# Kernel tuning notes

Hardware: AMD Instinct MI355X
Metric: run time of the kernel (lower is better)

## Reference

```python
import math
import jax, jax.numpy as jnp
import numpy as np

B, L, IN_DIM, D, OUT_DIM = 4, 4096, 512, 64, 512


def setup_inputs() -> dict:
    key = jax.random.key(0)
    ks = jax.random.split(key, 9)
    s_in = 1.0 / math.sqrt(IN_DIM)
    s_d = 1.0 / math.sqrt(D)
    return {
        "x": jax.random.normal(ks[0], (B, L, IN_DIM), jnp.float32),
        "Wq": jax.random.normal(ks[1], (IN_DIM, D), jnp.float32) * s_in,
        "bq": jax.random.normal(ks[2], (D,), jnp.float32) * s_in,
        "Wk": jax.random.normal(ks[3], (IN_DIM, D), jnp.float32) * s_in,
        "bk": jax.random.normal(ks[4], (D,), jnp.float32) * s_in,
        "Wv": jax.random.normal(ks[5], (IN_DIM, D), jnp.float32) * s_in,
        "bv": jax.random.normal(ks[6], (D,), jnp.float32) * s_in,
        "Wo": jax.random.normal(ks[7], (D, OUT_DIM), jnp.float32) * s_d,
        "bo": jax.random.normal(ks[8], (OUT_DIM,), jnp.float32) * s_d,
    }


def reference(x, Wq, bq, Wk, bk, Wv, bv, Wo, bo):
    # q, k, v: [B, L, D]
    q = x @ Wq + bq
    k = x @ Wk + bk
    v = x @ Wv + bv
    scale = 1.0 / math.sqrt(D)
    # scores: [B, Lq, Lk]
    scores = jnp.einsum("bqd,bkd->bqk", q, k) * scale
    # NOTE: original uses nn.Softmax(dim=1) -> softmax over the QUERY axis (axis=1)
    attention = jax.nn.softmax(scores, axis=1)
    values_with_attention = jnp.einsum("bqk,bkd->bqd", attention, v)
    output = values_with_attention @ Wo + bo
    return (output, attention)
```

## Files before the change

### kernel.cpp

```cpp
#include <hip/hip_runtime.h>
#include <hip/hip_fp16.h>
#include <math.h>

#define Bdim 4
#define Lseq 4096
#define INDIM 512
#define DH 64
#define OUTD 512
#define SCALE 0.125f
#define KSPL 8
#define QSPL 4
#define BL (Bdim * Lseq)

typedef _Float16 f16;
typedef _Float16 h8 __attribute__((ext_vector_type(8)));
typedef float f4 __attribute__((ext_vector_type(4)));

#define MFMA(a, b, c) __builtin_amdgcn_mfma_f32_16x16x32_f16(a, b, c, 0, 0, 0)

__global__ __launch_bounds__(256) void proj_h(const float* __restrict__ x,
                                              const float* __restrict__ W,
                                              const float* __restrict__ bias,
                                              f16* __restrict__ out, float scale) {
    __shared__ float xT[64 * 68];
    __shared__ float Ws[64 * 68];
    int t = threadIdx.x;
    int row0 = blockIdx.x * 64;
    int r4 = t >> 4;
    int c4 = t & 15;
    float acc[4][4] = {};
    for (int kc = 0; kc < INDIM; kc += 64) {
        __syncthreads();
        {
            int row = t >> 2, kq = (t & 3) * 16;
            const float4* src = (const float4*)(x + (size_t)(row0 + row) * INDIM + kc + kq);
            float tmp[16];
#pragma unroll
            for (int i = 0; i < 4; ++i) {
                float4 v = src[i];
                tmp[4*i+0] = v.x; tmp[4*i+1] = v.y; tmp[4*i+2] = v.z; tmp[4*i+3] = v.w;
            }
#pragma unroll
            for (int j = 0; j < 16; ++j) xT[(kq + j) * 68 + row] = tmp[j];
        }
        {
            int k = t >> 2, dq = (t & 3) * 16;
            const float4* src = (const float4*)(W + (size_t)(kc + k) * DH + dq);
#pragma unroll
            for (int i = 0; i < 4; ++i)
                *(float4*)(Ws + k * 68 + dq + 4 * i) = src[i];
        }
        __syncthreads();
#pragma unroll 8
        for (int k = 0; k < 64; ++k) {
            f4 xv = *(f4*)(xT + k * 68 + r4 * 4);
            f4 wv = *(f4*)(Ws + k * 68 + c4 * 4);
#pragma unroll
            for (int i = 0; i < 4; ++i)
#pragma unroll
                for (int j = 0; j < 4; ++j) acc[i][j] += xv[i] * wv[j];
        }
    }
#pragma unroll
    for (int i = 0; i < 4; ++i) {
        size_t row = row0 + r4 * 4 + i;
#pragma unroll
        for (int j = 0; j < 4; ++j) {
            int d = c4 * 4 + j;
            out[row * DH + d] = (f16)((acc[i][j] + bias[d]) * scale);
        }
    }
}

__global__ __launch_bounds__(256) void proj_f(const float* __restrict__ x,
                                              const float* __restrict__ W,
                                              const float* __restrict__ bias,
                                              float* __restrict__ out) {
    __shared__ float xT[64 * 68];
    __shared__ float Ws[64 * 68];
    int t = threadIdx.x;
    int row0 = blockIdx.x * 64;
    int r4 = t >> 4, c4 = t & 15;
    float acc[4][4] = {};
    for (int kc = 0; kc < INDIM; kc += 64) {
        __syncthreads();
        {
            int row = t >> 2, kq = (t & 3) * 16;
            const float4* src = (const float4*)(x + (size_t)(row0 + row) * INDIM + kc + kq);
            float tmp[16];
#pragma unroll
            for (int i = 0; i < 4; ++i) {
                float4 v = src[i];
                tmp[4*i+0] = v.x; tmp[4*i+1] = v.y; tmp[4*i+2] = v.z; tmp[4*i+3] = v.w;
            }
#pragma unroll
            for (int j = 0; j < 16; ++j) xT[(kq + j) * 68 + row] = tmp[j];
        }
        {
            int k = t >> 2, dq = (t & 3) * 16;
            const float4* src = (const float4*)(W + (size_t)(kc + k) * DH + dq);
#pragma unroll
            for (int i = 0; i < 4; ++i)
                *(float4*)(Ws + k * 68 + dq + 4 * i) = src[i];
        }
        __syncthreads();
#pragma unroll 8
        for (int k = 0; k < 64; ++k) {
            f4 xv = *(f4*)(xT + k * 68 + r4 * 4);
            f4 wv = *(f4*)(Ws + k * 68 + c4 * 4);
#pragma unroll
            for (int i = 0; i < 4; ++i)
#pragma unroll
                for (int j = 0; j < 4; ++j) acc[i][j] += xv[i] * wv[j];
        }
    }
#pragma unroll
    for (int i = 0; i < 4; ++i) {
        size_t row = row0 + r4 * 4 + i;
#pragma unroll
        for (int j = 0; j < 4; ++j) {
            int d = c4 * 4 + j;
            out[row * DH + d] = acc[i][j] + bias[d];
        }
    }
}

__global__ __launch_bounds__(256) void vtrans(const float* __restrict__ v32,
                                              f16* __restrict__ vt) {
    __shared__ float tile[64 * 65];
    int t = threadIdx.x;
    int b = blockIdx.y, k0 = blockIdx.x * 64;
#pragma unroll
    for (int i = 0; i < 4; ++i) {
        int lin = i * 256 + t;
        int row = lin >> 4, c4 = (lin & 15) * 4;
        float4 v = *(const float4*)(v32 + ((size_t)b * Lseq + k0 + row) * DH + c4);
        tile[row * 65 + c4 + 0] = v.x;
        tile[row * 65 + c4 + 1] = v.y;
        tile[row * 65 + c4 + 2] = v.z;
        tile[row * 65 + c4 + 3] = v.w;
    }
    __syncthreads();
    int d = t >> 2, kq = (t & 3) * 16;
#pragma unroll
    for (int i = 0; i < 2; ++i) {
        h8 pack;
#pragma unroll
        for (int j = 0; j < 8; ++j) pack[j] = (f16)tile[(kq + i * 8 + j) * 65 + d];
        *(h8*)(vt + ((size_t)b * DH + d) * Lseq + k0 + kq + i * 8) = pack;
    }
}

__global__ __launch_bounds__(256) void col_stats(const f16* __restrict__ qh,
                                                 const f16* __restrict__ kh,
                                                 float* __restrict__ lsum) {
    __shared__ __align__(16) f16 qlds[32 * 72];
    int t = threadIdx.x;
    int w = t >> 6, lane = t & 63;
    int l15 = lane & 15, quad = lane >> 4;
    int b = blockIdx.y;
    int kblk = blockIdx.x * 64;
    int qbase = blockIdx.z * (Lseq / QSPL);

    int krow = kblk + w * 16 + l15;
    const h8* kr = (const h8*)(kh + ((size_t)b * Lseq + krow) * DH + quad * 8);
    h8 a0 = kr[0];
    h8 a1 = kr[4];
    float lp[4] = {0.f, 0.f, 0.f, 0.f};

    for (int qs = 0; qs < Lseq / QSPL; qs += 32) {
        __syncthreads();
        {
            int row = t >> 3, c8 = t & 7;
            *(h8*)(qlds + row * 72 + c8 * 8) =
                *(const h8*)(qh + ((size_t)b * Lseq + qbase + qs + row) * DH + c8 * 8);
        }
        __syncthreads();
#pragma unroll
        for (int nt = 0; nt < 2; ++nt) {
            const f16* qp = qlds + (nt * 16 + l15) * 72 + quad * 8;
            h8 b0 = *(const h8*)qp;
            h8 b1 = *(const h8*)(qp + 32);
            f4 c = {0.f, 0.f, 0.f, 0.f};
            c = MFMA(a0, b0, c);
            c = MFMA(a1, b1, c);
#pragma unroll
            for (int reg = 0; reg < 4; ++reg) lp[reg] += __expf(c[reg]);
        }
    }
#pragma unroll
    for (int reg = 0; reg < 4; ++reg) {
        float v = lp[reg];
        v += __shfl_xor(v, 1);
        v += __shfl_xor(v, 2);
        v += __shfl_xor(v, 4);
        v += __shfl_xor(v, 8);
        if (l15 == 0)
            atomicAdd(&lsum[(size_t)b * Lseq + kblk + w * 16 + quad * 4 + reg], v);
    }
}

__global__ __launch_bounds__(256) void rlk(const float* __restrict__ lsum,
                                           float* __restrict__ rl) {
    int i = blockIdx.x * 256 + threadIdx.x;
    rl[i] = 1.0f / lsum[i];
}

__global__ __launch_bounds__(256) void attn_pv(const f16* __restrict__ qh,
                                               const f16* __restrict__ kh,
                                               const f16* __restrict__ vt,
                                               const float* __restrict__ rl,
                                               float* __restrict__ att,
                                               f16* __restrict__ opart) {
    __shared__ __align__(16) f16 klds[64 * 72];
    __shared__ __align__(16) f16 elds[4][32 * 80];
    int t = threadIdx.x;
    int w = t >> 6, lane = t & 63;
    int l15 = lane & 15, quad = lane >> 4;
    int b = blockIdx.y;
    int q0 = blockIdx.x * 128 + w * 32;
    int split = blockIdx.z;

    h8 aq[2][2];
#pragma unroll
    for (int mt = 0; mt < 2; ++mt) {
        const h8* qp = (const h8*)(qh + ((size_t)b * Lseq + q0 + mt * 16 + l15) * DH + quad * 8);
        aq[mt][0] = qp[0];
        aq[mt][1] = qp[4];
    }
    f4 o[2][4];
#pragma unroll
    for (int mt = 0; mt < 2; ++mt)
#pragma unroll
        for (int nt = 0; nt < 4; ++nt) o[mt][nt] = (f4){0.f, 0.f, 0.f, 0.f};

    const float* rlb = rl + (size_t)b * Lseq;
    f16* ew = elds[w];

    for (int kt = 0; kt < Lseq / KSPL; kt += 64) {
        int kbase = split * (Lseq / KSPL) + kt;
        __syncthreads();
#pragma unroll
        for (int i = 0; i < 2; ++i) {
            int lin = i * 256 + t;
            int row = lin >> 3, c8 = lin & 7;
            *(h8*)(klds + row * 72 + c8 * 8) =
                *(const h8*)(kh + ((size_t)b * Lseq + kbase + row) * DH + c8 * 8);
        }
        __syncthreads();

        h8 bk[4][2];
        float rlv[4];
#pragma unroll
        for (int nt = 0; nt < 4; ++nt) {
            const f16* kp = klds + (nt * 16 + l15) * 72 + quad * 8;
            bk[nt][0] = *(const h8*)kp;
            bk[nt][1] = *(const h8*)(kp + 32);
            rlv[nt] = rlb[kbase + nt * 16 + l15];
        }

#pragma unroll
        for (int mt = 0; mt < 2; ++mt)
#pragma unroll
            for (int nt = 0; nt < 4; ++nt) {
                f4 c = {0.f, 0.f, 0.f, 0.f};
                c = MFMA(aq[mt][0], bk[nt][0], c);
                c = MFMA(aq[mt][1], bk[nt][1], c);
#pragma unroll
                for (int reg = 0; reg < 4; ++reg) {
                    float a = __expf(c[reg]) * rlv[nt];
                    int qrow = mt * 16 + quad * 4 + reg;
                    att[((size_t)b * Lseq + q0 + qrow) * Lseq + kbase + nt * 16 + l15] = a;
                    ew[qrow * 80 + nt * 16 + l15] = (f16)a;
                }
            }

        h8 ae[2][2];
#pragma unroll
        for (int mt = 0; mt < 2; ++mt) {
            const f16* ep = ew + (mt * 16 + l15) * 80 + quad * 8;
            ae[mt][0] = *(const h8*)ep;
            ae[mt][1] = *(const h8*)(ep + 32);
        }
#pragma unroll
        for (int nt = 0; nt < 4; ++nt) {
            const h8* vp = (const h8*)(vt + ((size_t)b * DH + nt * 16 + l15) * Lseq + kbase + quad * 8);
            h8 bv0 = vp[0];
            h8 bv1 = vp[4];
            o[0][nt] = MFMA(ae[0][0], bv0, o[0][nt]);
            o[0][nt] = MFMA(ae[0][1], bv1, o[0][nt]);
            o[1][nt] = MFMA(ae[1][0], bv0, o[1][nt]);
            o[1][nt] = MFMA(ae[1][1], bv1, o[1][nt]);
        }
    }

#pragma unroll
    for (int mt = 0; mt < 2; ++mt)
#pragma unroll
        for (int nt = 0; nt < 4; ++nt)
#pragma unroll
            for (int reg = 0; reg < 4; ++reg) {
                size_t qrow = (size_t)b * Lseq + q0 + mt * 16 + quad * 4 + reg;
                opart[((size_t)split * BL + qrow) * DH + nt * 16 + l15] = (f16)o[mt][nt][reg];
            }
}

__global__ __launch_bounds__(256) void out_proj(const f16* __restrict__ opart,
                                                const float* __restrict__ Wo,
                                                const float* __restrict__ bo,
                                                float* __restrict__ out) {
    __shared__ float os[16 * DH];
    __shared__ float wos[DH * 128];
    int t = threadIdx.x;
    int rg = blockIdx.x, oq = blockIdx.y;
#pragma unroll
    for (int j = 0; j < 32; ++j) {
        int idx = j * 256 + t;
        int dd = idx >> 7, oo = idx & 127;
        wos[idx] = Wo[(size_t)dd * OUTD + oq * 128 + oo];
    }
#pragma unroll
    for (int j = 0; j < 4; ++j) {
        int idx = j * 256 + t;
        size_t R = (size_t)rg * 16 + (idx >> 6);
        int dd = idx & 63;
        float s = 0.f;
#pragma unroll
        for (int sp = 0; sp < KSPL; ++sp)
            s += (float)opart[((size_t)sp * BL + R) * DH + dd];
        os[idx] = s;
    }
    __syncthreads();
    int ol = t & 127, rp = t >> 7;
    float bias = bo[oq * 128 + ol];
#pragma unroll
    for (int j = 0; j < 8; ++j) {
        int rr = rp * 8 + j;
        float acc = bias;
#pragma unroll 16
        for (int dd = 0; dd < DH; ++dd) acc += os[rr * DH + dd] * wos[dd * 128 + ol];
        out[((size_t)rg * 16 + rr) * OUTD + oq * 128 + ol] = acc;
    }
}

extern "C" void kernel_launch(void* const* d_in, const int* in_sizes, int n_in,
                              void* d_out, int out_size, void* d_ws, size_t ws_size,
                              hipStream_t stream) {
    const float* x  = (const float*)d_in[0];
    const float* Wq = (const float*)d_in[1];
    const float* bq = (const float*)d_in[2];
    const float* Wk = (const float*)d_in[3];
    const float* bk = (const float*)d_in[4];
    const float* Wv = (const float*)d_in[5];
    const float* bv = (const float*)d_in[6];
    const float* Wo = (const float*)d_in[7];
    const float* bo = (const float*)d_in[8];

    float* out = (float*)d_out;
    float* att = out + (size_t)BL * OUTD;

    char* ws = (char*)d_ws;
    f16*   qh    = (f16*)(ws + 0);
    f16*   kh    = (f16*)(ws + (size_t)(2 << 20));
    float* v32   = (float*)(ws + (size_t)(4 << 20));
    f16*   vt    = (f16*)(ws + (size_t)(8 << 20));
    float* lsum  = (float*)(ws + (size_t)(10 << 20));
    float* rlw   = (float*)(ws + (size_t)(10 << 20) + (1 << 16));
    f16*   opart = (f16*)(ws + (size_t)(11 << 20));

    proj_h<<<dim3(BL / 64), 256, 0, stream>>>(x, Wq, bq, qh, SCALE);
    proj_h<<<dim3(BL / 64), 256, 0, stream>>>(x, Wk, bk, kh, 1.0f);
    proj_f<<<dim3(BL / 64), 256, 0, stream>>>(x, Wv, bv, v32);
    vtrans<<<dim3(Lseq / 64, Bdim), 256, 0, stream>>>(v32, vt);
    hipMemsetAsync(lsum, 0, (size_t)BL * sizeof(float), stream);
    col_stats<<<dim3(Lseq / 64, Bdim, QSPL), 256, 0, stream>>>(qh, kh, lsum);
    rlk<<<dim3(BL / 256), 256, 0, stream>>>(lsum, rlw);
    attn_pv<<<dim3(Lseq / 128, Bdim, KSPL), 256, 0, stream>>>(qh, kh, vt, rlw, att, opart);
    out_proj<<<dim3(BL / 16, 4), 256, 0, stream>>>(opart, Wo, bo, out);
}
```

Baseline: 522.4 us.

## Fuse QKV projection into one MFMA kernel, use exp2 and MFMA output projection

Replaces the three scalar fp32 projection kernels with a single fp16 MFMA kernel that reads x once and computes Q, K and V together, using transposed fp16 weight copies. Folds log2(e) into the Q scale so exp2f replaces __expf. Drops the LDS staging of K in attn_pv and col_stats. Swaps the operand order so attention rows are written as float4 stores. Also converts the output projection to MFMA and sums the split partials in fp16. The cost is extra small weight-transpose launches and more fp16 rounding in the projections and the partial reduction.

New measurement: 523.0 us. About the same (+0.1%).

```diff
diff --git a/kernel.cpp b/kernel.cpp
--- a/kernel.cpp
+++ b/kernel.cpp
@@ -1,5 +1,4 @@
 #include <hip/hip_runtime.h>
-#include <hip/hip_fp16.h>
 #include <math.h>
 
 #define Bdim 4
@@ -7,196 +6,139 @@
 #define INDIM 512
 #define DH 64
 #define OUTD 512
-#define SCALE 0.125f
 #define KSPL 8
 #define QSPL 4
 #define BL (Bdim * Lseq)
+#define QS 0.18033688011112042f
 
 typedef _Float16 f16;
 typedef _Float16 h8 __attribute__((ext_vector_type(8)));
+typedef _Float16 h4 __attribute__((ext_vector_type(4)));
 typedef float f4 __attribute__((ext_vector_type(4)));
 
 #define MFMA(a, b, c) __builtin_amdgcn_mfma_f32_16x16x32_f16(a, b, c, 0, 0, 0)
 
-__global__ __launch_bounds__(256) void proj_h(const float* __restrict__ x,
-                                              const float* __restrict__ W,
-                                              const float* __restrict__ bias,
-                                              f16* __restrict__ out, float scale) {
-    __shared__ float xT[64 * 68];
-    __shared__ float Ws[64 * 68];
+__global__ __launch_bounds__(256) void transpose_w(const float* __restrict__ W,
+                                                   f16* __restrict__ WT,
+                                                   int K, int N, float scale) {
+    int id = blockIdx.x * 256 + threadIdx.x;
+    if (id >= K * N) return;
+    int n = id / K, k = id % K;
+    WT[(size_t)n * K + k] = (f16)(W[(size_t)k * N + n] * scale);
+}
+
+__global__ __launch_bounds__(256) void qkvh(const float* __restrict__ x,
+                                            const f16* __restrict__ WqT,
+                                            const f16* __restrict__ WkT,
+                                            const f16* __restrict__ WvT,
+                                            const float* __restrict__ bq,
+                                            const float* __restrict__ bk,
+                                            const float* __restrict__ bv,
+                                            f16* __restrict__ qh,
+                                            f16* __restrict__ kh,
+                                            f16* __restrict__ vh) {
+    __shared__ __align__(16) f16 xh[64 * 136];
     int t = threadIdx.x;
-    int row0 = blockIdx.x * 64;
-    int r4 = t >> 4;
-    int c4 = t & 15;
-    float acc[4][4] = {};
-    for (int kc = 0; kc < INDIM; kc += 64) {
+    int w = t >> 6, lane = t & 63, l15 = lane & 15, quad = lane >> 4;
+    size_t row0 = (size_t)blockIdx.x * 64;
+
+    f4 acc[12];
+#pragma unroll
+    for (int i = 0; i < 12; ++i) acc[i] = (f4){0.f, 0.f, 0.f, 0.f};
+
+    const f16* wbase[12];
+#pragma unroll
+    for (int nt = 0; nt < 12; ++nt) {
+        const f16* Wt = nt < 4 ? WqT : (nt < 8 ? WkT : WvT);
+        wbase[nt] = Wt + (size_t)((nt & 3) * 16 + l15) * INDIM + quad * 8;
+    }
+
+    int xr = t >> 2, xc = (t & 3) * 4;
+    for (int kc = 0; kc < INDIM; kc += 128) {
         __syncthreads();
-        {
-            int row = t >> 2, kq = (t & 3) * 16;
-            const float4* src = (const float4*)(x + (size_t)(row0 + row) * INDIM + kc + kq);
-            float tmp[16];
-#pragma unroll
-            for (int i = 0; i < 4; ++i) {
-                float4 v = src[i];
-                tmp[4*i+0] = v.x; tmp[4*i+1] = v.y; tmp[4*i+2] = v.z; tmp[4*i+3] = v.w;
+#pragma unroll
+        for (int i = 0; i < 8; ++i) {
+            float4 v = *(const float4*)(x + (row0 + xr) * INDIM + kc + xc + i * 16);
+            h4 p = {(f16)v.x, (f16)v.y, (f16)v.z, (f16)v.w};
+            *(h4*)(xh + xr * 136 + xc + i * 16) = p;
+        }
+        __syncthreads();
+#pragma unroll
+        for (int ks = 0; ks < 4; ++ks) {
+            h8 a = *(const h8*)(xh + (w * 16 + l15) * 136 + ks * 32 + quad * 8);
+#pragma unroll
+            for (int nt = 0; nt < 12; ++nt) {
+                h8 bf = *(const h8*)(wbase[nt] + kc + ks * 32);
+                acc[nt] = MFMA(a, bf, acc[nt]);
             }
-#pragma unroll
-            for (int j = 0; j < 16; ++j) xT[(kq + j) * 68 + row] = tmp[j];
-        }
-        {
-            int k = t >> 2, dq = (t & 3) * 16;
-            const float4* src = (const float4*)(W + (size_t)(kc + k) * DH + dq);
-#pragma unroll
-            for (int i = 0; i < 4; ++i)
-                *(float4*)(Ws + k * 68 + dq + 4 * i) = src[i];
-        }
-        __syncthreads();
-#pragma unroll 8
-        for (int k = 0; k < 64; ++k) {
-            f4 xv = *(f4*)(xT + k * 68 + r4 * 4);
-            f4 wv = *(f4*)(Ws + k * 68 + c4 * 4);
-#pragma unroll
-            for (int i = 0; i < 4; ++i)
-#pragma unroll
-                for (int j = 0; j < 4; ++j) acc[i][j] += xv[i] * wv[j];
-        }
-    }
-#pragma unroll
-    for (int i = 0; i < 4; ++i) {
-        size_t row = row0 + r4 * 4 + i;
-#pragma unroll
-        for (int j = 0; j < 4; ++j) {
-            int d = c4 * 4 + j;
-            out[row * DH + d] = (f16)((acc[i][j] + bias[d]) * scale);
-        }
-    }
-}
-
-__global__ __launch_bounds__(256) void proj_f(const float* __restrict__ x,
-                                              const float* __restrict__ W,
-                                              const float* __restrict__ bias,
-                                              float* __restrict__ out) {
-    __shared__ float xT[64 * 68];
-    __shared__ float Ws[64 * 68];
-    int t = threadIdx.x;
-    int row0 = blockIdx.x * 64;
-    int r4 = t >> 4, c4 = t & 15;
-    float acc[4][4] = {};
-    for (int kc = 0; kc < INDIM; kc += 64) {
-        __syncthreads();
-        {
-            int row = t >> 2, kq = (t & 3) * 16;
-            const float4* src = (const float4*)(x + (size_t)(row0 + row) * INDIM + kc + kq);
-            float tmp[16];
-#pragma unroll
-            for (int i = 0; i < 4; ++i) {
-                float4 v = src[i];
-                tmp[4*i+0] = v.x; tmp[4*i+1] = v.y; tmp[4*i+2] = v.z; tmp[4*i+3] = v.w;
-            }
-#pragma unroll
-            for (int j = 0; j < 16; ++j) xT[(kq + j) * 68 + row] = tmp[j];
-        }
-        {
-            int k = t >> 2, dq = (t & 3) * 16;
-            const float4* src = (const float4*)(W + (size_t)(kc + k) * DH + dq);
-#pragma unroll
-            for (int i = 0; i < 4; ++i)
-                *(float4*)(Ws + k * 68 + dq + 4 * i) = src[i];
-        }
-        __syncthreads();
-#pragma unroll 8
-        for (int k = 0; k < 64; ++k) {
-            f4 xv = *(f4*)(xT + k * 68 + r4 * 4);
-            f4 wv = *(f4*)(Ws + k * 68 + c4 * 4);
-#pragma unroll
-            for (int i = 0; i < 4; ++i)
-#pragma unroll
-                for (int j = 0; j < 4; ++j) acc[i][j] += xv[i] * wv[j];
-        }
-    }
-#pragma unroll
-    for (int i = 0; i < 4; ++i) {
-        size_t row = row0 + r4 * 4 + i;
-#pragma unroll
-        for (int j = 0; j < 4; ++j) {
-            int d = c4 * 4 + j;
-            out[row * DH + d] = acc[i][j] + bias[d];
-        }
-    }
-}
-
-__global__ __launch_bounds__(256) void vtrans(const float* __restrict__ v32,
+        }
+    }
+#pragma unroll
+    for (int nt = 0; nt < 12; ++nt) {
+        int n = (nt & 3) * 16 + l15;
+        f16* dst;
+        float bias;
+        if (nt < 4)      { dst = qh; bias = bq[n] * QS; }
+        else if (nt < 8) { dst = kh; bias = bk[n]; }
+        else             { dst = vh; bias = bv[n]; }
+#pragma unroll
+        for (int r = 0; r < 4; ++r) {
+            size_t row = row0 + w * 16 + quad * 4 + r;
+            dst[row * DH + n] = (f16)(acc[nt][r] + bias);
+        }
+    }
+}
+
+__global__ __launch_bounds__(256) void vtrans(const f16* __restrict__ vh,
                                               f16* __restrict__ vt) {
-    __shared__ float tile[64 * 65];
+    __shared__ __align__(16) f16 tile[64 * 72];
     int t = threadIdx.x;
     int b = blockIdx.y, k0 = blockIdx.x * 64;
-#pragma unroll
-    for (int i = 0; i < 4; ++i) {
-        int lin = i * 256 + t;
-        int row = lin >> 4, c4 = (lin & 15) * 4;
-        float4 v = *(const float4*)(v32 + ((size_t)b * Lseq + k0 + row) * DH + c4);
-        tile[row * 65 + c4 + 0] = v.x;
-        tile[row * 65 + c4 + 1] = v.y;
-        tile[row * 65 + c4 + 2] = v.z;
-        tile[row * 65 + c4 + 3] = v.w;
-    }
+    int row = t >> 2, c16 = (t & 3) * 16;
+    const h8* src = (const h8*)(vh + ((size_t)b * Lseq + k0 + row) * DH + c16);
+    *(h8*)(tile + row * 72 + c16) = src[0];
+    *(h8*)(tile + row * 72 + c16 + 8) = src[1];
     __syncthreads();
     int d = t >> 2, kq = (t & 3) * 16;
 #pragma unroll
     for (int i = 0; i < 2; ++i) {
-        h8 pack;
-#pragma unroll
-        for (int j = 0; j < 8; ++j) pack[j] = (f16)tile[(kq + i * 8 + j) * 65 + d];
-        *(h8*)(vt + ((size_t)b * DH + d) * Lseq + k0 + kq + i * 8) = pack;
+        h8 p;
+#pragma unroll
+        for (int j = 0; j < 8; ++j) p[j] = tile[(kq + i * 8 + j) * 72 + d];
+        *(h8*)(vt + ((size_t)b * DH + d) * Lseq + k0 + kq + i * 8) = p;
     }
 }
 
 __global__ __launch_bounds__(256) void col_stats(const f16* __restrict__ qh,
                                                  const f16* __restrict__ kh,
                                                  float* __restrict__ lsum) {
-    __shared__ __align__(16) f16 qlds[32 * 72];
-    int t = threadIdx.x;
-    int w = t >> 6, lane = t & 63;
-    int l15 = lane & 15, quad = lane >> 4;
+    int t = threadIdx.x, w = t >> 6, lane = t & 63, l15 = lane & 15, quad = lane >> 4;
     int b = blockIdx.y;
-    int kblk = blockIdx.x * 64;
-    int qbase = blockIdx.z * (Lseq / QSPL);
-
-    int krow = kblk + w * 16 + l15;
-    const h8* kr = (const h8*)(kh + ((size_t)b * Lseq + krow) * DH + quad * 8);
-    h8 a0 = kr[0];
-    h8 a1 = kr[4];
-    float lp[4] = {0.f, 0.f, 0.f, 0.f};
-
-    for (int qs = 0; qs < Lseq / QSPL; qs += 32) {
-        __syncthreads();
-        {
-            int row = t >> 3, c8 = t & 7;
-            *(h8*)(qlds + row * 72 + c8 * 8) =
-                *(const h8*)(qh + ((size_t)b * Lseq + qbase + qs + row) * DH + c8 * 8);
-        }
-        __syncthreads();
-#pragma unroll
-        for (int nt = 0; nt < 2; ++nt) {
-            const f16* qp = qlds + (nt * 16 + l15) * 72 + quad * 8;
-            h8 b0 = *(const h8*)qp;
-            h8 b1 = *(const h8*)(qp + 32);
-            f4 c = {0.f, 0.f, 0.f, 0.f};
-            c = MFMA(a0, b0, c);
-            c = MFMA(a1, b1, c);
-#pragma unroll
-            for (int reg = 0; reg < 4; ++reg) lp[reg] += __expf(c[reg]);
-        }
-    }
-#pragma unroll
-    for (int reg = 0; reg < 4; ++reg) {
-        float v = lp[reg];
+    int k16 = blockIdx.x * 64 + w * 16;
+    size_t qbase = (size_t)blockIdx.z * (Lseq / QSPL);
+
+    const h8* kr = (const h8*)(kh + ((size_t)b * Lseq + k16 + l15) * DH + quad * 8);
+    h8 a0 = kr[0], a1 = kr[4];
+    f4 lp = {0.f, 0.f, 0.f, 0.f};
+    const f16* qb = qh + ((size_t)b * Lseq + qbase) * DH;
+#pragma unroll 4
+    for (int q = 0; q < Lseq / QSPL; q += 16) {
+        const h8* qr = (const h8*)(qb + (size_t)(q + l15) * DH + quad * 8);
+        h8 b0 = qr[0], b1 = qr[4];
+        f4 c = {0.f, 0.f, 0.f, 0.f};
+        c = MFMA(a0, b0, c);
+        c = MFMA(a1, b1, c);
+#pragma unroll
+        for (int r = 0; r < 4; ++r) lp[r] += exp2f(c[r]);
+    }
+#pragma unroll
+    for (int r = 0; r < 4; ++r) {
+        float v = lp[r];
         v += __shfl_xor(v, 1);
         v += __shfl_xor(v, 2);
         v += __shfl_xor(v, 4);
         v += __shfl_xor(v, 8);
-        if (l15 == 0)
-            atomicAdd(&lsum[(size_t)b * Lseq + kblk + w * 16 + quad * 4 + reg], v);
+        if (l15 == 0) atomicAdd(&lsum[(size_t)b * Lseq + k16 + quad * 4 + r], v);
     }
 }
 
@@ -212,21 +154,17 @@
                                                const float* __restrict__ rl,
                                                float* __restrict__ att,
                                                f16* __restrict__ opart) {
-    __shared__ __align__(16) f16 klds[64 * 72];
-    __shared__ __align__(16) f16 elds[4][32 * 80];
-    int t = threadIdx.x;
-    int w = t >> 6, lane = t & 63;
-    int l15 = lane & 15, quad = lane >> 4;
-    int b = blockIdx.y;
+    __shared__ __align__(16) f16 ew[4][32 * 72];
+    int t = threadIdx.x, w = t >> 6, lane = t & 63, l15 = lane & 15, quad = lane >> 4;
+    int b = blockIdx.y, split = blockIdx.z;
     int q0 = blockIdx.x * 128 + w * 32;
-    int split = blockIdx.z;
-
-    h8 aq[2][2];
+
+    h8 bq[2][2];
 #pragma unroll
     for (int mt = 0; mt < 2; ++mt) {
         const h8* qp = (const h8*)(qh + ((size_t)b * Lseq + q0 + mt * 16 + l15) * DH + quad * 8);
-        aq[mt][0] = qp[0];
-        aq[mt][1] = qp[4];
+        bq[mt][0] = qp[0];
+        bq[mt][1] = qp[4];
     }
     f4 o[2][4];
 #pragma unroll
@@ -234,112 +172,95 @@
 #pragma unroll
         for (int nt = 0; nt < 4; ++nt) o[mt][nt] = (f4){0.f, 0.f, 0.f, 0.f};
 
+    f16* e = ew[w];
+    const f16* khb = kh + (size_t)b * Lseq * DH;
+    const f16* vtb = vt + (size_t)b * DH * Lseq;
     const float* rlb = rl + (size_t)b * Lseq;
-    f16* ew = elds[w];
+    float* attb = att + ((size_t)b * Lseq + q0) * Lseq;
 
     for (int kt = 0; kt < Lseq / KSPL; kt += 64) {
-        int kbase = split * (Lseq / KSPL) + kt;
-        __syncthreads();
-#pragma unroll
-        for (int i = 0; i < 2; ++i) {
-            int lin = i * 256 + t;
-            int row = lin >> 3, c8 = lin & 7;
-            *(h8*)(klds + row * 72 + c8 * 8) =
-                *(const h8*)(kh + ((size_t)b * Lseq + kbase + row) * DH + c8 * 8);
-        }
-        __syncthreads();
-
-        h8 bk[4][2];
-        float rlv[4];
+        int kb = split * (Lseq / KSPL) + kt;
+        h8 ak[4][2];
+        f4 rlv[4];
 #pragma unroll
         for (int nt = 0; nt < 4; ++nt) {
-            const f16* kp = klds + (nt * 16 + l15) * 72 + quad * 8;
-            bk[nt][0] = *(const h8*)kp;
-            bk[nt][1] = *(const h8*)(kp + 32);
-            rlv[nt] = rlb[kbase + nt * 16 + l15];
-        }
-
+            const h8* kp = (const h8*)(khb + (size_t)(kb + nt * 16 + l15) * DH + quad * 8);
+            ak[nt][0] = kp[0];
+            ak[nt][1] = kp[4];
+            rlv[nt] = *(const f4*)(rlb + kb + nt * 16 + quad * 4);
+        }
 #pragma unroll
         for (int mt = 0; mt < 2; ++mt)
 #pragma unroll
             for (int nt = 0; nt < 4; ++nt) {
                 f4 c = {0.f, 0.f, 0.f, 0.f};
-                c = MFMA(aq[mt][0], bk[nt][0], c);
-                c = MFMA(aq[mt][1], bk[nt][1], c);
-#pragma unroll
-                for (int reg = 0; reg < 4; ++reg) {
-                    float a = __expf(c[reg]) * rlv[nt];
-                    int qrow = mt * 16 + quad * 4 + reg;
-                    att[((size_t)b * Lseq + q0 + qrow) * Lseq + kbase + nt * 16 + l15] = a;
-                    ew[qrow * 80 + nt * 16 + l15] = (f16)a;
+                c = MFMA(ak[nt][0], bq[mt][0], c);
+                c = MFMA(ak[nt][1], bq[mt][1], c);
+                f4 av;
+                h4 ah;
+#pragma unroll
+                for (int r = 0; r < 4; ++r) {
+                    float a = exp2f(c[r]) * rlv[nt][r];
+                    av[r] = a;
+                    ah[r] = (f16)a;
                 }
+                *(f4*)(attb + (size_t)(mt * 16 + l15) * Lseq + kb + nt * 16 + quad * 4) = av;
+                *(h4*)(e + (mt * 16 + l15) * 72 + nt * 16 + quad * 4) = ah;
             }
-
         h8 ae[2][2];
 #pragma unroll
         for (int mt = 0; mt < 2; ++mt) {
-            const f16* ep = ew + (mt * 16 + l15) * 80 + quad * 8;
+            const f16* ep = e + (mt * 16 + l15) * 72 + quad * 8;
             ae[mt][0] = *(const h8*)ep;
             ae[mt][1] = *(const h8*)(ep + 32);
         }
 #pragma unroll
         for (int nt = 0; nt < 4; ++nt) {
-            const h8* vp = (const h8*)(vt + ((size_t)b * DH + nt * 16 + l15) * Lseq + kbase + quad * 8);
-            h8 bv0 = vp[0];
-            h8 bv1 = vp[4];
-            o[0][nt] = MFMA(ae[0][0], bv0, o[0][nt]);
-            o[0][nt] = MFMA(ae[0][1], bv1, o[0][nt]);
-            o[1][nt] = MFMA(ae[1][0], bv0, o[1][nt]);
-            o[1][nt] = MFMA(ae[1][1], bv1, o[1][nt]);
-        }
-    }
-
+            const h8* vp = (const h8*)(vtb + (size_t)(nt * 16 + l15) * Lseq + kb + quad * 8);
+            h8 b0 = vp[0], b1 = vp[4];
+#pragma unroll
+            for (int mt = 0; mt < 2; ++mt) {
+                o[mt][nt] = MFMA(ae[mt][0], b0, o[mt][nt]);
+                o[mt][nt] = MFMA(ae[mt][1], b1, o[mt][nt]);
+            }
+        }
+    }
 #pragma unroll
     for (int mt = 0; mt < 2; ++mt)
 #pragma unroll
         for (int nt = 0; nt < 4; ++nt)
 #pragma unroll
-            for (int reg = 0; reg < 4; ++reg) {
-                size_t qrow = (size_t)b * Lseq + q0 + mt * 16 + quad * 4 + reg;
-                opart[((size_t)split * BL + qrow) * DH + nt * 16 + l15] = (f16)o[mt][nt][reg];
+            for (int r = 0; r < 4; ++r) {
+                size_t qrow = (size_t)b * Lseq + q0 + mt * 16 + quad * 4 + r;
+                opart[((size_t)split * BL + qrow) * DH + nt * 16 + l15] = (f16)o[mt][nt][r];
             }
 }
 
-__global__ __launch_bounds__(256) void out_proj(const f16* __restrict__ opart,
-                                                const float* __restrict__ Wo,
-                                                const float* __restrict__ bo,
-                                                float* __restrict__ out) {
-    __shared__ float os[16 * DH];
-    __shared__ float wos[DH * 128];
-    int t = threadIdx.x;
-    int rg = blockIdx.x, oq = blockIdx.y;
-#pragma unroll
-    for (int j = 0; j < 32; ++j) {
-        int idx = j * 256 + t;
-        int dd = idx >> 7, oo = idx & 127;
-        wos[idx] = Wo[(size_t)dd * OUTD + oq * 128 + oo];
-    }
-#pragma unroll
-    for (int j = 0; j < 4; ++j) {
-        int idx = j * 256 + t;
-        size_t R = (size_t)rg * 16 + (idx >> 6);
-        int dd = idx & 63;
-        float s = 0.f;
-#pragma unroll
-        for (int sp = 0; sp < KSPL; ++sp)
-            s += (float)opart[((size_t)sp * BL + R) * DH + dd];
-        os[idx] = s;
-    }
-    __syncthreads();
-    int ol = t & 127, rp = t >> 7;
-    float bias = bo[oq * 128 + ol];
-#pragma unroll
-    for (int j = 0; j < 8; ++j) {
-        int rr = rp * 8 + j;
-        float acc = bias;
-#pragma unroll 16
-        for (int dd = 0; dd < DH; ++dd) acc += os[rr * DH + dd] * wos[dd * 128 + ol];
-        out[((size_t)rg * 16 + rr) * OUTD + oq * 128 + ol] = acc;
+__global__ __launch_bounds__(256) void oproj(const f16* __restrict__ opart,
+                                             const f16* __restrict__ WoT,
+                                             const float* __restrict__ bo,
+                                             float* __restrict__ out) {
+    int t = threadIdx.x, w = t >> 6, lane = t & 63, l15 = lane & 15, quad = lane >> 4;
+    size_t row0 = (size_t)blockIdx.x * 64 + w * 16;
+
+    h8 a0 = (h8)(f16)0.f, a1 = (h8)(f16)0.f;
+#pragma unroll
+    for (int sp = 0; sp < KSPL; ++sp) {
+        const h8* op = (const h8*)(opart + ((size_t)sp * BL + row0 + l15) * DH + quad * 8);
+        a0 += op[0];
+        a1 += op[4];
+    }
+#pragma unroll
+    for (int nt = 0; nt < OUTD / 16; ++nt) {
+        const h8* wp = (const h8*)(WoT + (size_t)(nt * 16 + l15) * DH + quad * 8);
+        h8 b0 = wp[0], b1 = wp[4];
+        f4 c = {0.f, 0.f, 0.f, 0.f};
+        c = MFMA(a0, b0, c);
+        c = MFMA(a1, b1, c);
+        float bias = bo[nt * 16 + l15];
+#pragma unroll
+        for (int r = 0; r < 4; ++r)
+            out[(row0 + quad * 4 + r) * OUTD + nt * 16 + l15] = c[r] + bias;
     }
 }
 
@@ -360,21 +281,27 @@
     float* att = out + (size_t)BL * OUTD;
 
     char* ws = (char*)d_ws;
-    f16*   qh    = (f16*)(ws + 0);
-    f16*   kh    = (f16*)(ws + (size_t)(2 << 20));
-    float* v32   = (float*)(ws + (size_t)(4 << 20));
-    f16*   vt    = (f16*)(ws + (size_t)(8 << 20));
-    float* lsum  = (float*)(ws + (size_t)(10 << 20));
-    float* rlw   = (float*)(ws + (size_t)(10 << 20) + (1 << 16));
-    f16*   opart = (f16*)(ws + (size_t)(11 << 20));
-
-    proj_h<<<dim3(BL / 64), 256, 0, stream>>>(x, Wq, bq, qh, SCALE);
-    proj_h<<<dim3(BL / 64), 256, 0, stream>>>(x, Wk, bk, kh, 1.0f);
-    proj_f<<<dim3(BL / 64), 256, 0, stream>>>(x, Wv, bv, v32);
-    vtrans<<<dim3(Lseq / 64, Bdim), 256, 0, stream>>>(v32, vt);
+    f16*   qh   = (f16*)(ws);
+    f16*   kh   = (f16*)(ws + (size_t)(2 << 20));
+    f16*   vh   = (f16*)(ws + (size_t)(4 << 20));
+    f16*   vt   = (f16*)(ws + (size_t)(6 << 20));
+    f16*   WqT  = (f16*)(ws + (size_t)(8 << 20));
+    f16*   WkT  = (f16*)(ws + (size_t)(8 << 20) + (1 << 16));
+    f16*   WvT  = (f16*)(ws + (size_t)(8 << 20) + (2 << 16));
+    f16*   WoT  = (f16*)(ws + (size_t)(8 << 20) + (3 << 16));
+    float* lsum = (float*)(ws + (size_t)(8 << 20) + (4 << 16));
+    float* rlw  = (float*)(ws + (size_t)(8 << 20) + (5 << 16));
+    f16*   opart = (f16*)(ws + (size_t)(9 << 20));
+
+    transpose_w<<<dim3(128), 256, 0, stream>>>(Wq, WqT, INDIM, DH, QS);
+    transpose_w<<<dim3(128), 256, 0, stream>>>(Wk, WkT, INDIM, DH, 1.0f);
+    transpose_w<<<dim3(128), 256, 0, stream>>>(Wv, WvT, INDIM, DH, 1.0f);
+    transpose_w<<<dim3(128), 256, 0, stream>>>(Wo, WoT, DH, OUTD, 1.0f);
+    qkvh<<<dim3(BL / 64), 256, 0, stream>>>(x, WqT, WkT, WvT, bq, bk, bv, qh, kh, vh);
+    vtrans<<<dim3(Lseq / 64, Bdim), 256, 0, stream>>>(vh, vt);
     hipMemsetAsync(lsum, 0, (size_t)BL * sizeof(float), stream);
     col_stats<<<dim3(Lseq / 64, Bdim, QSPL), 256, 0, stream>>>(qh, kh, lsum);
     rlk<<<dim3(BL / 256), 256, 0, stream>>>(lsum, rlw);
     attn_pv<<<dim3(Lseq / 128, Bdim, KSPL), 256, 0, stream>>>(qh, kh, vt, rlw, att, opart);
-    out_proj<<<dim3(BL / 16, 4), 256, 0, stream>>>(opart, Wo, bo, out);
-}
+    oproj<<<dim3(BL / 64), 256, 0, stream>>>(opart, WoT, bo, out);
+}
```
